# Kernel optimization log

Measured on AMD Instinct MI355X. Metric: run time of the kernel, lower is better.

Reference implementation:

```python
import jax, jax.numpy as jnp
import numpy as np

T, B, D, H = 512, 64, 256, 256


def setup_inputs() -> dict:
    key = jax.random.key(0)
    ks = jax.random.split(key, 14)
    w = lambda k, shp: (0.01 * jax.random.normal(k, shp, dtype=jnp.float32))
    return {
        "X": jax.random.normal(ks[0], (T, B, D), dtype=jnp.float32),
        "Wa_x": w(ks[1], (D, H)), "Wi_x": w(ks[2], (D, H)),
        "Wf_x": w(ks[3], (D, H)), "Wo_x": w(ks[4], (D, H)),
        "Wa_h": w(ks[5], (H, H)), "Wi_h": w(ks[6], (H, H)),
        "Wf_h": w(ks[7], (H, H)), "Wo_h": w(ks[8], (H, H)),
        "ba": w(ks[9], (H,)), "bi": w(ks[10], (H,)),
        "bf": w(ks[11], (H,)), "bo": w(ks[12], (H,)),
    }


def reference(X, Wa_x, Wi_x, Wf_x, Wo_x, Wa_h, Wi_h, Wf_h, Wo_h, ba, bi, bf, bo):
    # Fuse the four gate input projections into one big GEMM over all timesteps.
    # Gate order: a (cell candidate, tanh), i, f, o (sigmoid).
    h_dim = Wa_h.shape[0]
    Wx = jnp.concatenate([Wa_x, Wi_x, Wf_x, Wo_x], axis=1)      # [D, 4H]
    Wh = jnp.concatenate([Wa_h, Wi_h, Wf_h, Wo_h], axis=1)      # [H, 4H]
    b = jnp.concatenate([ba, bi, bf, bo])                        # [4H]
    gx = jnp.einsum('tbd,dg->tbg', X, Wx) + b                    # [T, B, 4H]

    def step(carry, g):
        h, s = carry
        g = g + h @ Wh                                           # [B, 4H]
        a = jnp.tanh(g[:, :h_dim])
        i = jax.nn.sigmoid(g[:, h_dim:2 * h_dim])
        f = jax.nn.sigmoid(g[:, 2 * h_dim:3 * h_dim])
        o = jax.nn.sigmoid(g[:, 3 * h_dim:])
        # t==0 in the original omits h/s terms, equivalent to h0 = s0 = 0
        s = a * i + s * f
        h = jnp.tanh(s) * o
        return (h, s), h

    bsz = X.shape[1]
    h0 = jnp.zeros((bsz, h_dim), dtype=X.dtype)
    s0 = jnp.zeros((bsz, h_dim), dtype=X.dtype)
    _, outputs = jax.lax.scan(step, (h0, s0), gx)                # [T, B, H]
    return outputs
```

## Files before the change

### kernel.cpp

```cpp
#include <hip/hip_runtime.h>
#include <hip/hip_fp16.h>


#define T_STEPS 512
#define BATCH   64
#define HID     256
#define G4      1024
#define GM      (T_STEPS * BATCH)

typedef _Float16 half2_t __attribute__((ext_vector_type(2)));
typedef _Float16 f16x8   __attribute__((ext_vector_type(8)));
typedef float    f32x4   __attribute__((ext_vector_type(4)));

#define XH_OFF  0u
#define WXT_OFF 8388608u
#define GX_OFF  8912896u
#define WH8_BYTE_OFF (8650752u * 2u)

__device__ __forceinline__ float fast_sigmoid(float x) {
    return 1.0f / (1.0f + __expf(-x));
}
__device__ __forceinline__ float fast_tanh(float x) {
    return 2.0f / (1.0f + __expf(-2.0f * x)) - 1.0f;
}

__device__ __forceinline__ unsigned char sw_e4m3(float x) {
    unsigned u = __float_as_uint(x);
    unsigned s = (u >> 24) & 0x80u;
    int e = (int)((u >> 23) & 0xffu) - 127;
    unsigned m = u & 0x7fffffu;
    if (e < -6) return (unsigned char)s;
    m += 0x00080000u;
    if (m & 0x800000u) { m = 0; e += 1; }
    int E = e + 7;
    if (E > 15 || (E == 15 && (m >> 20) > 6)) { E = 15; m = 6u << 20; }
    return (unsigned char)(s | ((unsigned)E << 3) | (m >> 20));
}
template <bool HI>
__device__ __forceinline__ unsigned cvt2_fp8(float a, float b, unsigned old) {
#if __has_builtin(__builtin_amdgcn_cvt_pk_fp8_f32)
    return (unsigned)__builtin_amdgcn_cvt_pk_fp8_f32(a, b, (int)old, HI);
#else
    unsigned lo16 = (unsigned)sw_e4m3(a) | ((unsigned)sw_e4m3(b) << 8);
    return HI ? ((old & 0xFFFFu) | (lo16 << 16))
              : ((old & 0xFFFF0000u) | lo16);
#endif
}

__global__ __launch_bounds__(256) void k_prep_x(const float* __restrict__ X,
                                                _Float16* __restrict__ Xh) {
    const int i = blockIdx.x * 256 + threadIdx.x;
    float4 v = ((const float4*)X)[i];
    half2_t a; a.x = (_Float16)v.x; a.y = (_Float16)v.y;
    half2_t b; b.x = (_Float16)v.z; b.y = (_Float16)v.w;
    ((half2_t*)Xh)[2 * i]     = a;
    ((half2_t*)Xh)[2 * i + 1] = b;
}

__global__ __launch_bounds__(256) void k_prep_w(
    const float* __restrict__ Wax, const float* __restrict__ Wix,
    const float* __restrict__ Wfx, const float* __restrict__ Wox,
    _Float16* __restrict__ Wxt)
{
    const int id = blockIdx.x * 256 + threadIdx.x;
    const int k  = id >> 10;
    const int c  = id & 1023;
    const int g  = c >> 8;
    const int j  = c & 255;
    const float* src = (g == 0) ? Wax : (g == 1) ? Wix : (g == 2) ? Wfx : Wox;
    Wxt[c * 256 + k] = (_Float16)src[k * 256 + j];
}

__global__ __launch_bounds__(256) void k_prep_wfrag8(
    const float* __restrict__ Wah, const float* __restrict__ Wih,
    const float* __restrict__ Wfh, const float* __restrict__ Woh,
    unsigned char* __restrict__ Wh8)
{
    const int id  = blockIdx.x * 256 + threadIdx.x;
    const int l   = id & 63;
    const int kt  = (id >> 6) & 7;
    const int ntG = id >> 9;
    const int c   = ntG * 16 + (l & 15);
    const int u   = c >> 2;
    const int g   = c & 3;
    const int k0  = kt * 32 + (l >> 4) * 8;
    const float* W = (g == 0) ? Wah : (g == 1) ? Wih : (g == 2) ? Wfh : Woh;
    float v[8];
#pragma unroll
    for (int e = 0; e < 8; ++e)
        v[e] = W[(size_t)(k0 + e) * 256 + u] * 64.0f;
    unsigned lo = cvt2_fp8<false>(v[0], v[1], 0u);
    lo = cvt2_fp8<true>(v[2], v[3], lo);
    unsigned hi = cvt2_fp8<false>(v[4], v[5], 0u);
    hi = cvt2_fp8<true>(v[6], v[7], hi);
    uint2 pk; pk.x = lo; pk.y = hi;
    *(uint2*)(Wh8 + ((size_t)(ntG * 8 + kt) * 64 + l) * 8) = pk;
}

__global__ __launch_bounds__(256) void k_gemm(const _Float16* __restrict__ Xh,
                                              const _Float16* __restrict__ Wxt,
                                              const float* __restrict__ ba,
                                              const float* __restrict__ bi,
                                              const float* __restrict__ bf_,
                                              const float* __restrict__ bo,
                                              _Float16* __restrict__ gx)
{
    const int lane = threadIdx.x & 63, wave = threadIdx.x >> 6;
    const int rowbase = blockIdx.x * 128 + wave * 32;
    const int colbase = blockIdx.y * 64;
    const int r15 = lane & 15, kg = lane >> 4;

    f32x4 acc[2][4] = {};
    const _Float16* ap0 = Xh  + (size_t)(rowbase + r15) * 256 + kg * 8;
    const _Float16* ap1 = ap0 + 16 * 256;
    const _Float16* bp  = Wxt + (size_t)(colbase + r15) * 256 + kg * 8;

#pragma unroll
    for (int ks = 0; ks < 8; ++ks) {
        f16x8 a0 = *(const f16x8*)(ap0 + ks * 32);
        f16x8 a1 = *(const f16x8*)(ap1 + ks * 32);
        f16x8 b0 = *(const f16x8*)(bp  + ks * 32);
        f16x8 b1 = *(const f16x8*)(bp  + 16 * 256 + ks * 32);
        f16x8 b2 = *(const f16x8*)(bp  + 32 * 256 + ks * 32);
        f16x8 b3 = *(const f16x8*)(bp  + 48 * 256 + ks * 32);
        acc[0][0] = __builtin_amdgcn_mfma_f32_16x16x32_f16(a0, b0, acc[0][0], 0, 0, 0);
        acc[0][1] = __builtin_amdgcn_mfma_f32_16x16x32_f16(a0, b1, acc[0][1], 0, 0, 0);
        acc[0][2] = __builtin_amdgcn_mfma_f32_16x16x32_f16(a0, b2, acc[0][2], 0, 0, 0);
        acc[0][3] = __builtin_amdgcn_mfma_f32_16x16x32_f16(a0, b3, acc[0][3], 0, 0, 0);
        acc[1][0] = __builtin_amdgcn_mfma_f32_16x16x32_f16(a1, b0, acc[1][0], 0, 0, 0);
        acc[1][1] = __builtin_amdgcn_mfma_f32_16x16x32_f16(a1, b1, acc[1][1], 0, 0, 0);
        acc[1][2] = __builtin_amdgcn_mfma_f32_16x16x32_f16(a1, b2, acc[1][2], 0, 0, 0);
        acc[1][3] = __builtin_amdgcn_mfma_f32_16x16x32_f16(a1, b3, acc[1][3], 0, 0, 0);
    }
    float bias_n[4];
#pragma unroll
    for (int nt = 0; nt < 4; ++nt) {
        int col = colbase + nt * 16 + r15;
        bias_n[nt] = (col < 256) ? ba[col]
                   : (col < 512) ? bi[col - 256]
                   : (col < 768) ? bf_[col - 512]
                                 : bo[col - 768];
    }
#pragma unroll
    for (int mt = 0; mt < 2; ++mt)
#pragma unroll
        for (int nt = 0; nt < 4; ++nt)
#pragma unroll
            for (int r = 0; r < 4; ++r) {
                int row = rowbase + mt * 16 + kg * 4 + r;
                int col = colbase + nt * 16 + r15;
                gx[(size_t)row * G4 + col] = (_Float16)(acc[mt][nt][r] + bias_n[nt]);
            }
}


#define M8(a, bfr, acc) \
    __builtin_amdgcn_mfma_f32_16x16x32_fp8_fp8((a), (bfr), (acc), 0, 0, 0)
#define WB(n, k) (*(const long*)(Wp + ((size_t)((n) * 8 + (k)) * 64) * 8))

#define DB(n)                                                                  \
    long b##n##_0 = WB(n,0), b##n##_1 = WB(n,1), b##n##_2 = WB(n,2),           \
         b##n##_3 = WB(n,3), b##n##_4 = WB(n,4), b##n##_5 = WB(n,5),           \
         b##n##_6 = WB(n,6), b##n##_7 = WB(n,7);

#define TILE(n)                                                                \
    {                                                                          \
        f32x4 acc = {0.f, 0.f, 0.f, 0.f};                                      \
        acc = M8(a0, b##n##_0, acc); acc = M8(a1, b##n##_1, acc);              \
        acc = M8(a2, b##n##_2, acc); acc = M8(a3, b##n##_3, acc);              \
        acc = M8(a4, b##n##_4, acc); acc = M8(a5, b##n##_5, acc);              \
        acc = M8(a6, b##n##_6, acc); acc = M8(a7, b##n##_7, acc);              \
        if (lane < 16) actw[(n) * 16 + lane] = acc[0];                         \
    }

__global__ void __launch_bounds__(256, 1)
__attribute__((amdgpu_waves_per_eu(1, 1)))
k_recur(const unsigned char* __restrict__ Wh8, const _Float16* __restrict__ gx,
        float* __restrict__ out)
{
    const int b    = blockIdx.x;
    const int tid  = threadIdx.x;
    const int lane = tid & 63;
    const int w    = tid >> 6;

    __shared__ __align__(16) float act[1024];
    __shared__ __align__(8)  unsigned char hbufs[2][256];

    float* actw = act + w * 256;
    const unsigned char* Wp = Wh8 + ((size_t)(w * 16) * 8 * 64) * 8 + lane * 8;

    DB(0)  DB(1)  DB(2)  DB(3)  DB(4)  DB(5)  DB(6)  DB(7)
    DB(8)  DB(9)  DB(10) DB(11) DB(12) DB(13) DB(14) DB(15)

    hbufs[0][tid] = 0;
    float s = 0.0f;
    const int u = w * 64 + lane;
    _Float16 gc0 = gx[(size_t)b * G4 + u];
    _Float16 gc1 = gx[(size_t)b * G4 + 256 + u];
    _Float16 gc2 = gx[(size_t)b * G4 + 512 + u];
    _Float16 gc3 = gx[(size_t)b * G4 + 768 + u];
    __syncthreads();

#pragma unroll 1
    for (int t = 0; t < T_STEPS; ++t) {
        _Float16 gn0 = (_Float16)0.f, gn1 = (_Float16)0.f;
        _Float16 gn2 = (_Float16)0.f, gn3 = (_Float16)0.f;
        if (t + 1 < T_STEPS) {
            const size_t r = ((size_t)(t + 1) * BATCH + b) * G4;
            gn0 = gx[r + u];       gn1 = gx[r + 256 + u];
            gn2 = gx[r + 512 + u]; gn3 = gx[r + 768 + u];
        }

        const unsigned char* hb = &hbufs[t & 1][0] + ((lane >> 4) * 8);
        long a0 = *(const long*)(hb + 0);
        long a1 = *(const long*)(hb + 32);
        long a2 = *(const long*)(hb + 64);
        long a3 = *(const long*)(hb + 96);
        long a4 = *(const long*)(hb + 128);
        long a5 = *(const long*)(hb + 160);
        long a6 = *(const long*)(hb + 192);
        long a7 = *(const long*)(hb + 224);

        TILE(0)  TILE(1)  TILE(2)  TILE(3)
        TILE(4)  TILE(5)  TILE(6)  TILE(7)
        TILE(8)  TILE(9)  TILE(10) TILE(11)
        TILE(12) TILE(13) TILE(14) TILE(15)

        asm volatile("s_waitcnt lgkmcnt(0)" ::: "memory");

        {
            float4 g4v = ((const float4*)act)[w * 64 + lane];
            const float S = 0.0009765625f;
            float gA = g4v.x * S + (float)gc0;
            float gB = g4v.y * S + (float)gc1;
            float gC = g4v.z * S + (float)gc2;
            float gD = g4v.w * S + (float)gc3;
            float aa = fast_tanh(gA);
            float ii = fast_sigmoid(gB);
            float ff = fast_sigmoid(gC);
            float oo = fast_sigmoid(gD);
            s = aa * ii + s * ff;
            float h = fast_tanh(s) * oo;
            out[((size_t)t * BATCH + b) * HID + u] = h;
            unsigned p8 = cvt2_fp8<false>(h * 16.0f, h * 16.0f, 0u);
            hbufs[(t + 1) & 1][u] = (unsigned char)(p8 & 0xffu);
        }
        gc0 = gn0; gc1 = gn1; gc2 = gn2; gc3 = gn3;
        __syncthreads();
    }
}

extern "C" void kernel_launch(void* const* d_in, const int* in_sizes, int n_in,
                              void* d_out, int out_size, void* d_ws, size_t ws_size,
                              hipStream_t stream) {
    const float* X   = (const float*)d_in[0];
    const float* Wax = (const float*)d_in[1];
    const float* Wix = (const float*)d_in[2];
    const float* Wfx = (const float*)d_in[3];
    const float* Wox = (const float*)d_in[4];
    const float* Wah = (const float*)d_in[5];
    const float* Wih = (const float*)d_in[6];
    const float* Wfh = (const float*)d_in[7];
    const float* Woh = (const float*)d_in[8];
    const float* ba  = (const float*)d_in[9];
    const float* bi  = (const float*)d_in[10];
    const float* bf  = (const float*)d_in[11];
    const float* bo  = (const float*)d_in[12];

    _Float16* ws  = (_Float16*)d_ws;
    _Float16* Xh  = ws + XH_OFF;
    _Float16* Wxt = ws + WXT_OFF;
    _Float16* gxp = ws + GX_OFF;
    unsigned char* Wh8 = (unsigned char*)d_ws + WH8_BYTE_OFF;

    k_prep_x<<<dim3(GM * 256 / 4 / 256), dim3(256), 0, stream>>>(X, Xh);
    k_prep_w<<<dim3(1024), dim3(256), 0, stream>>>(Wax, Wix, Wfx, Wox, Wxt);
    k_prep_wfrag8<<<dim3(128), dim3(256), 0, stream>>>(Wah, Wih, Wfh, Woh, Wh8);
    k_gemm<<<dim3(GM / 128, G4 / 64), dim3(256), 0, stream>>>(
        Xh, Wxt, ba, bi, bf, bo, gxp);
    k_recur<<<dim3(BATCH), dim3(256), 0, stream>>>(Wh8, gxp, (float*)d_out);
}
```

Before: 1.027 ms.

## Interleave recurrent MFMA chains across tiles and interleave gx gates per unit

The recurrent loop now issues its MFMAs k-step by k-step across all 16 output tiles, using 16 independent accumulators, instead of running each tile's 8-deep dependent chain one after another. This is meant to hide MFMA latency. The input-projection kernel now writes gx with the four gates interleaved per hidden unit, so each thread fetches its next-step gate inputs with one 8-byte load instead of four scattered 2-byte loads. The cost is higher accumulator register pressure (64 extra VGPRs) on top of the 128 registers of preloaded weights.

Measured after the change: 929.4 us. 1.1x faster.

```diff
diff --git a/kernel.cpp b/kernel.cpp
--- a/kernel.cpp
+++ b/kernel.cpp
@@ -149,7 +149,9 @@
             for (int r = 0; r < 4; ++r) {
                 int row = rowbase + mt * 16 + kg * 4 + r;
                 int col = colbase + nt * 16 + r15;
-                gx[(size_t)row * G4 + col] = (_Float16)(acc[mt][nt][r] + bias_n[nt]);
+                int g   = col >> 8, j = col & 255;
+                gx[(size_t)row * G4 + 4 * j + g] =
+                    (_Float16)(acc[mt][nt][r] + bias_n[nt]);
             }
 }
 
@@ -163,15 +165,15 @@
          b##n##_3 = WB(n,3), b##n##_4 = WB(n,4), b##n##_5 = WB(n,5),           \
          b##n##_6 = WB(n,6), b##n##_7 = WB(n,7);
 
-#define TILE(n)                                                                \
-    {                                                                          \
-        f32x4 acc = {0.f, 0.f, 0.f, 0.f};                                      \
-        acc = M8(a0, b##n##_0, acc); acc = M8(a1, b##n##_1, acc);              \
-        acc = M8(a2, b##n##_2, acc); acc = M8(a3, b##n##_3, acc);              \
-        acc = M8(a4, b##n##_4, acc); acc = M8(a5, b##n##_5, acc);              \
-        acc = M8(a6, b##n##_6, acc); acc = M8(a7, b##n##_7, acc);              \
-        if (lane < 16) actw[(n) * 16 + lane] = acc[0];                         \
-    }
+#define KSTEP(k)                                                               \
+    c0  = M8(a##k, b0_##k,  c0);  c1  = M8(a##k, b1_##k,  c1);                 \
+    c2  = M8(a##k, b2_##k,  c2);  c3  = M8(a##k, b3_##k,  c3);                 \
+    c4  = M8(a##k, b4_##k,  c4);  c5  = M8(a##k, b5_##k,  c5);                 \
+    c6  = M8(a##k, b6_##k,  c6);  c7  = M8(a##k, b7_##k,  c7);                 \
+    c8  = M8(a##k, b8_##k,  c8);  c9  = M8(a##k, b9_##k,  c9);                 \
+    c10 = M8(a##k, b10_##k, c10); c11 = M8(a##k, b11_##k, c11);                \
+    c12 = M8(a##k, b12_##k, c12); c13 = M8(a##k, b13_##k, c13);                \
+    c14 = M8(a##k, b14_##k, c14); c15 = M8(a##k, b15_##k, c15);
 
 __global__ void __launch_bounds__(256, 1)
 __attribute__((amdgpu_waves_per_eu(1, 1)))
@@ -195,20 +197,14 @@
     hbufs[0][tid] = 0;
     float s = 0.0f;
     const int u = w * 64 + lane;
-    _Float16 gc0 = gx[(size_t)b * G4 + u];
-    _Float16 gc1 = gx[(size_t)b * G4 + 256 + u];
-    _Float16 gc2 = gx[(size_t)b * G4 + 512 + u];
-    _Float16 gc3 = gx[(size_t)b * G4 + 768 + u];
+    uint2 gcu = *(const uint2*)(gx + (size_t)b * G4 + 4 * u);
     __syncthreads();
 
 #pragma unroll 1
     for (int t = 0; t < T_STEPS; ++t) {
-        _Float16 gn0 = (_Float16)0.f, gn1 = (_Float16)0.f;
-        _Float16 gn2 = (_Float16)0.f, gn3 = (_Float16)0.f;
+        uint2 gnx; gnx.x = 0u; gnx.y = 0u;
         if (t + 1 < T_STEPS) {
-            const size_t r = ((size_t)(t + 1) * BATCH + b) * G4;
-            gn0 = gx[r + u];       gn1 = gx[r + 256 + u];
-            gn2 = gx[r + 512 + u]; gn3 = gx[r + 768 + u];
+            gnx = *(const uint2*)(gx + ((size_t)(t + 1) * BATCH + b) * G4 + 4 * u);
         }
 
         const unsigned char* hb = &hbufs[t & 1][0] + ((lane >> 4) * 8);
@@ -221,20 +217,36 @@
         long a6 = *(const long*)(hb + 192);
         long a7 = *(const long*)(hb + 224);
 
-        TILE(0)  TILE(1)  TILE(2)  TILE(3)
-        TILE(4)  TILE(5)  TILE(6)  TILE(7)
-        TILE(8)  TILE(9)  TILE(10) TILE(11)
-        TILE(12) TILE(13) TILE(14) TILE(15)
-
+        f32x4 c0  = {0,0,0,0}, c1  = {0,0,0,0}, c2  = {0,0,0,0}, c3  = {0,0,0,0};
+        f32x4 c4  = {0,0,0,0}, c5  = {0,0,0,0}, c6  = {0,0,0,0}, c7  = {0,0,0,0};
+        f32x4 c8  = {0,0,0,0}, c9  = {0,0,0,0}, c10 = {0,0,0,0}, c11 = {0,0,0,0};
+        f32x4 c12 = {0,0,0,0}, c13 = {0,0,0,0}, c14 = {0,0,0,0}, c15 = {0,0,0,0};
+
+        KSTEP(0) KSTEP(1) KSTEP(2) KSTEP(3)
+        KSTEP(4) KSTEP(5) KSTEP(6) KSTEP(7)
+
+        if (lane < 16) {
+            actw[0  * 16 + lane] = c0[0];   actw[1  * 16 + lane] = c1[0];
+            actw[2  * 16 + lane] = c2[0];   actw[3  * 16 + lane] = c3[0];
+            actw[4  * 16 + lane] = c4[0];   actw[5  * 16 + lane] = c5[0];
+            actw[6  * 16 + lane] = c6[0];   actw[7  * 16 + lane] = c7[0];
+            actw[8  * 16 + lane] = c8[0];   actw[9  * 16 + lane] = c9[0];
+            actw[10 * 16 + lane] = c10[0];  actw[11 * 16 + lane] = c11[0];
+            actw[12 * 16 + lane] = c12[0];  actw[13 * 16 + lane] = c13[0];
+            actw[14 * 16 + lane] = c14[0];  actw[15 * 16 + lane] = c15[0];
+        }
         asm volatile("s_waitcnt lgkmcnt(0)" ::: "memory");
 
         {
+            half2_t p01, p23;
+            __builtin_memcpy(&p01, &gcu.x, 4);
+            __builtin_memcpy(&p23, &gcu.y, 4);
             float4 g4v = ((const float4*)act)[w * 64 + lane];
             const float S = 0.0009765625f;
-            float gA = g4v.x * S + (float)gc0;
-            float gB = g4v.y * S + (float)gc1;
-            float gC = g4v.z * S + (float)gc2;
-            float gD = g4v.w * S + (float)gc3;
+            float gA = g4v.x * S + (float)p01.x;
+            float gB = g4v.y * S + (float)p01.y;
+            float gC = g4v.z * S + (float)p23.x;
+            float gD = g4v.w * S + (float)p23.y;
             float aa = fast_tanh(gA);
             float ii = fast_sigmoid(gB);
             float ff = fast_sigmoid(gC);
@@ -245,7 +257,7 @@
             unsigned p8 = cvt2_fp8<false>(h * 16.0f, h * 16.0f, 0u);
             hbufs[(t + 1) & 1][u] = (unsigned char)(p8 & 0xffu);
         }
-        gc0 = gn0; gc1 = gn1; gc2 = gn2; gc3 = gn3;
+        gcu = gnx;
         __syncthreads();
     }
 }
```
